# Kernel optimization log

Hardware: AMD Instinct MI355X
Metric: run time of the kernel (lower is better)

## Reference

```python
import jax, jax.numpy as jnp
import numpy as np


def setup_inputs() -> dict:
    key = jax.random.key(0)
    k1, k2 = jax.random.split(key)
    x = jax.random.normal(k1, (32, 112, 112, 64), dtype=jnp.float32)
    kernels = jax.random.normal(k2, (3, 3, 64, 128), dtype=jnp.float32) * 0.05
    biases = jnp.zeros((128,), dtype=jnp.float32)
    return {"x": x, "kernels": kernels, "biases": biases}


def reference(x, kernels, biases):
    # Stride-1 VALID cross-correlation, NHWC input, HWIO kernel -> NHWC output.
    # Matches the original's per-pixel sum(patch * kernel) over all input channels.
    out = jax.lax.conv_general_dilated(
        x, kernels,
        window_strides=(1, 1),
        padding="VALID",
        dimension_numbers=("NHWC", "HWIO", "NHWC"),
    )
    out = out + biases  # broadcast over (B, H_out, W_out, F)
    return jax.nn.relu(out)  # activation=relu per init_kwargs
```

## Files before the change

kernel.cpp:

```cpp
#include <hip/hip_runtime.h>
#include <hip/hip_bf16.h>

typedef __attribute__((ext_vector_type(4))) float f32x4;
typedef __attribute__((ext_vector_type(8))) short bf16x8;
typedef __attribute__((ext_vector_type(8))) unsigned short u16x8;

#define NB 32
#define HH 112
#define WW 112
#define CIN 64
#define COUT 128
#define HOUT 110
#define WOUT 110

__device__ __forceinline__ unsigned short f2bf(float f) {
  unsigned int x = __float_as_uint(f);
  x += 0x7fffu + ((x >> 16) & 1u);
  return (unsigned short)(x >> 16);
}

__global__ void prepack_b_kernel(const float* __restrict__ kern,
                                 unsigned short* __restrict__ bt) {
  int idx = blockIdx.x * 256 + threadIdx.x;
  if (idx >= 576 * COUT) return;
  int co = idx / 576;
  int k = idx - co * 576;
  bt[idx] = f2bf(kern[k * COUT + co]);
}

template <bool PREPACK>
__global__ __launch_bounds__(512)
void conv_mfma_kernel(const float* __restrict__ x,
                      const void* __restrict__ bsrc,
                      const float* __restrict__ bias,
                      float* __restrict__ out) {
  __shared__ __align__(16) unsigned short As[128 * 64];
  __shared__ __align__(16) unsigned short Bs[128 * 64];

  const int tid = threadIdx.x;
  const int m0 = blockIdx.x * 128;

  const int sr = tid >> 2;
  const int sc = tid & 3;
  const int m = m0 + sr;
  const int wo = m % WOUT;
  const int t1 = m / WOUT;
  const int ho = t1 % HOUT;
  const int b = t1 / HOUT;
  const float* xrow = x + (((b * HH) + ho) * WW + wo) * CIN + sc * 16;
  const int swzS = (sr & 7) << 4;
  unsigned short* aw0 = As + sr * 64 + ((((sc * 32) + 0) ^ swzS) >> 1);
  unsigned short* aw1 = As + sr * 64 + ((((sc * 32) + 16) ^ swzS) >> 1);

  const unsigned short* btrow = nullptr;
  unsigned short* bw0 = nullptr;
  unsigned short* bw1 = nullptr;
  if constexpr (PREPACK) {
    btrow = (const unsigned short*)bsrc + sr * 576 + sc * 16;
    bw0 = Bs + sr * 64 + ((((sc * 32) + 0) ^ swzS) >> 1);
    bw1 = Bs + sr * 64 + ((((sc * 32) + 16) ^ swzS) >> 1);
  }
  const int bci = tid >> 3;
  const int bco = (tid & 7) * 16;

  const int lane = tid & 63;
  const int wid = tid >> 6;
  const int wm = wid >> 1;
  const int wn = wid & 1;
  const int l16 = lane & 15;
  const int lk = lane >> 4;
  const int swzR = (l16 & 7) << 4;

  f32x4 acc[2][4];
#pragma unroll
  for (int i = 0; i < 2; ++i)
#pragma unroll
    for (int j = 0; j < 4; ++j)
      acc[i][j] = (f32x4){0.f, 0.f, 0.f, 0.f};

  const unsigned short* ar0 = As + (wm * 32 + 0 + l16) * 64;
  const unsigned short* ar1 = As + (wm * 32 + 16 + l16) * 64;
  const unsigned short* br0 = Bs + (wn * 64 + 0 + l16) * 64;
  const unsigned short* br1 = Bs + (wn * 64 + 16 + l16) * 64;
  const unsigned short* br2 = Bs + (wn * 64 + 32 + l16) * 64;
  const unsigned short* br3 = Bs + (wn * 64 + 48 + l16) * 64;

  for (int kk = 0; kk < 9; ++kk) {
    const int kh = kk / 3;
    const int kw = kk - kh * 3;

    __syncthreads();

    {
      const float* src = xrow + (kh * WW + kw) * CIN;
      f32x4 f0 = *(const f32x4*)(src + 0);
      f32x4 f1 = *(const f32x4*)(src + 4);
      f32x4 f2 = *(const f32x4*)(src + 8);
      f32x4 f3 = *(const f32x4*)(src + 12);
      u16x8 v0, v1;
#pragma unroll
      for (int j = 0; j < 4; ++j) {
        v0[j]     = f2bf(f0[j]);
        v0[4 + j] = f2bf(f1[j]);
        v1[j]     = f2bf(f2[j]);
        v1[4 + j] = f2bf(f3[j]);
      }
      *(u16x8*)aw0 = v0;
      *(u16x8*)aw1 = v1;
    }

    if constexpr (PREPACK) {
      const u16x8* p = (const u16x8*)(btrow + kk * 64);
      *(u16x8*)bw0 = p[0];
      *(u16x8*)bw1 = p[1];
    } else {
      const float* kern = (const float*)bsrc;
      const float* ks = kern + (kk * 64 + bci) * COUT + bco;
      f32x4 g0 = *(const f32x4*)(ks + 0);
      f32x4 g1 = *(const f32x4*)(ks + 4);
      f32x4 g2 = *(const f32x4*)(ks + 8);
      f32x4 g3 = *(const f32x4*)(ks + 12);
#pragma unroll
      for (int j = 0; j < 4; ++j) {
        int c0 = bco + j;
        Bs[c0 * 64 + (((bci * 2) ^ ((c0 & 7) << 4)) >> 1)] = f2bf(g0[j]);
        int c1 = bco + 4 + j;
        Bs[c1 * 64 + (((bci * 2) ^ ((c1 & 7) << 4)) >> 1)] = f2bf(g1[j]);
        int c2 = bco + 8 + j;
        Bs[c2 * 64 + (((bci * 2) ^ ((c2 & 7) << 4)) >> 1)] = f2bf(g2[j]);
        int c3 = bco + 12 + j;
        Bs[c3 * 64 + (((bci * 2) ^ ((c3 & 7) << 4)) >> 1)] = f2bf(g3[j]);
      }
    }

    __syncthreads();

#pragma unroll
    for (int ks = 0; ks < 2; ++ks) {
      const int cbs = ((ks * 64 + lk * 16) ^ swzR) >> 1;
      bf16x8 a0 = *(const bf16x8*)(ar0 + cbs);
      bf16x8 a1 = *(const bf16x8*)(ar1 + cbs);
      bf16x8 b0 = *(const bf16x8*)(br0 + cbs);
      bf16x8 b1 = *(const bf16x8*)(br1 + cbs);
      bf16x8 b2 = *(const bf16x8*)(br2 + cbs);
      bf16x8 b3 = *(const bf16x8*)(br3 + cbs);
      acc[0][0] = __builtin_amdgcn_mfma_f32_16x16x32_bf16(a0, b0, acc[0][0], 0, 0, 0);
      acc[0][1] = __builtin_amdgcn_mfma_f32_16x16x32_bf16(a0, b1, acc[0][1], 0, 0, 0);
      acc[0][2] = __builtin_amdgcn_mfma_f32_16x16x32_bf16(a0, b2, acc[0][2], 0, 0, 0);
      acc[0][3] = __builtin_amdgcn_mfma_f32_16x16x32_bf16(a0, b3, acc[0][3], 0, 0, 0);
      acc[1][0] = __builtin_amdgcn_mfma_f32_16x16x32_bf16(a1, b0, acc[1][0], 0, 0, 0);
      acc[1][1] = __builtin_amdgcn_mfma_f32_16x16x32_bf16(a1, b1, acc[1][1], 0, 0, 0);
      acc[1][2] = __builtin_amdgcn_mfma_f32_16x16x32_bf16(a1, b2, acc[1][2], 0, 0, 0);
      acc[1][3] = __builtin_amdgcn_mfma_f32_16x16x32_bf16(a1, b3, acc[1][3], 0, 0, 0);
    }
  }

  const int ncol = wn * 64 + l16;
  const float bv0 = bias[ncol + 0];
  const float bv1 = bias[ncol + 16];
  const float bv2 = bias[ncol + 32];
  const float bv3 = bias[ncol + 48];
  const int mrow0 = m0 + wm * 32 + lk * 4;
#pragma unroll
  for (int mf = 0; mf < 2; ++mf) {
#pragma unroll
    for (int j = 0; j < 4; ++j) {
      const int row = mrow0 + mf * 16 + j;
      float* orow = out + (size_t)row * COUT + ncol;
      orow[0]  = fmaxf(acc[mf][0][j] + bv0, 0.f);
      orow[16] = fmaxf(acc[mf][1][j] + bv1, 0.f);
      orow[32] = fmaxf(acc[mf][2][j] + bv2, 0.f);
      orow[48] = fmaxf(acc[mf][3][j] + bv3, 0.f);
    }
  }
}

extern "C" void kernel_launch(void* const* d_in, const int* in_sizes, int n_in,
                              void* d_out, int out_size, void* d_ws, size_t ws_size,
                              hipStream_t stream) {
  const float* x = (const float*)d_in[0];
  const float* kern = (const float*)d_in[1];
  const float* bias = (const float*)d_in[2];
  float* out = (float*)d_out;

  const size_t bt_bytes = 576 * COUT * sizeof(unsigned short);
  if (d_ws != nullptr && ws_size >= bt_bytes) {
    unsigned short* bt = (unsigned short*)d_ws;
    prepack_b_kernel<<<288, 256, 0, stream>>>(kern, bt);
    conv_mfma_kernel<true><<<3025, 512, 0, stream>>>(x, (const void*)bt, bias, out);
  } else {
    conv_mfma_kernel<false><<<3025, 512, 0, stream>>>(x, (const void*)kern, bias, out);
  }
}
```

Measured before the change: 114.8 us.

## Double-buffer LDS tiles and prefetch next tap's loads during MFMA

Splits the A and B shared-memory tiles into two buffers and issues the global loads for the next kernel tap before the MFMA block on the current tap. The next buffer is converted and stored after the compute, leaving one barrier per iteration instead of two. The aim is to hide global load latency behind matrix math. In exchange it doubles LDS use to 64KB per block and raises register pressure, which may lower occupancy.

Result: faster. 110.4 us (-3.9%).

```diff
diff --git a/kernel.cpp b/kernel.cpp
--- a/kernel.cpp
+++ b/kernel.cpp
@@ -12,6 +12,7 @@
 #define COUT 128
 #define HOUT 110
 #define WOUT 110
+#define NWG 3025
 
 __device__ __forceinline__ unsigned short f2bf(float f) {
   unsigned int x = __float_as_uint(f);
@@ -34,8 +35,8 @@
                       const void* __restrict__ bsrc,
                       const float* __restrict__ bias,
                       float* __restrict__ out) {
-  __shared__ __align__(16) unsigned short As[128 * 64];
-  __shared__ __align__(16) unsigned short Bs[128 * 64];
+  __shared__ __align__(16) unsigned short As[2][128 * 64];
+  __shared__ __align__(16) unsigned short Bs[2][128 * 64];
 
   const int tid = threadIdx.x;
   const int m0 = blockIdx.x * 128;
@@ -49,16 +50,12 @@
   const int b = t1 / HOUT;
   const float* xrow = x + (((b * HH) + ho) * WW + wo) * CIN + sc * 16;
   const int swzS = (sr & 7) << 4;
-  unsigned short* aw0 = As + sr * 64 + ((((sc * 32) + 0) ^ swzS) >> 1);
-  unsigned short* aw1 = As + sr * 64 + ((((sc * 32) + 16) ^ swzS) >> 1);
+  const int awoff0 = sr * 64 + ((((sc * 32) + 0) ^ swzS) >> 1);
+  const int awoff1 = sr * 64 + ((((sc * 32) + 16) ^ swzS) >> 1);
 
   const unsigned short* btrow = nullptr;
-  unsigned short* bw0 = nullptr;
-  unsigned short* bw1 = nullptr;
   if constexpr (PREPACK) {
     btrow = (const unsigned short*)bsrc + sr * 576 + sc * 16;
-    bw0 = Bs + sr * 64 + ((((sc * 32) + 0) ^ swzS) >> 1);
-    bw1 = Bs + sr * 64 + ((((sc * 32) + 16) ^ swzS) >> 1);
   }
   const int bci = tid >> 3;
   const int bco = (tid & 7) * 16;
@@ -71,6 +68,13 @@
   const int lk = lane >> 4;
   const int swzR = (l16 & 7) << 4;
 
+  const int aroff0 = (wm * 32 + 0 + l16) * 64;
+  const int aroff1 = (wm * 32 + 16 + l16) * 64;
+  const int broff0 = (wn * 64 + 0 + l16) * 64;
+  const int broff1 = (wn * 64 + 16 + l16) * 64;
+  const int broff2 = (wn * 64 + 32 + l16) * 64;
+  const int broff3 = (wn * 64 + 48 + l16) * 64;
+
   f32x4 acc[2][4];
 #pragma unroll
   for (int i = 0; i < 2; ++i)
@@ -78,72 +82,82 @@
     for (int j = 0; j < 4; ++j)
       acc[i][j] = (f32x4){0.f, 0.f, 0.f, 0.f};
 
-  const unsigned short* ar0 = As + (wm * 32 + 0 + l16) * 64;
-  const unsigned short* ar1 = As + (wm * 32 + 16 + l16) * 64;
-  const unsigned short* br0 = Bs + (wn * 64 + 0 + l16) * 64;
-  const unsigned short* br1 = Bs + (wn * 64 + 16 + l16) * 64;
-  const unsigned short* br2 = Bs + (wn * 64 + 32 + l16) * 64;
-  const unsigned short* br3 = Bs + (wn * 64 + 48 + l16) * 64;
-
-  for (int kk = 0; kk < 9; ++kk) {
-    const int kh = kk / 3;
-    const int kw = kk - kh * 3;
-
-    __syncthreads();
-
-    {
-      const float* src = xrow + (kh * WW + kw) * CIN;
-      f32x4 f0 = *(const f32x4*)(src + 0);
-      f32x4 f1 = *(const f32x4*)(src + 4);
-      f32x4 f2 = *(const f32x4*)(src + 8);
-      f32x4 f3 = *(const f32x4*)(src + 12);
-      u16x8 v0, v1;
-#pragma unroll
-      for (int j = 0; j < 4; ++j) {
-        v0[j]     = f2bf(f0[j]);
-        v0[4 + j] = f2bf(f1[j]);
-        v1[j]     = f2bf(f2[j]);
-        v1[4 + j] = f2bf(f3[j]);
-      }
-      *(u16x8*)aw0 = v0;
-      *(u16x8*)aw1 = v1;
-    }
-
+  {
+    f32x4 f0 = *(const f32x4*)(xrow + 0);
+    f32x4 f1 = *(const f32x4*)(xrow + 4);
+    f32x4 f2 = *(const f32x4*)(xrow + 8);
+    f32x4 f3 = *(const f32x4*)(xrow + 12);
+    u16x8 v0, v1;
+#pragma unroll
+    for (int j = 0; j < 4; ++j) {
+      v0[j]     = f2bf(f0[j]);
+      v0[4 + j] = f2bf(f1[j]);
+      v1[j]     = f2bf(f2[j]);
+      v1[4 + j] = f2bf(f3[j]);
+    }
+    *(u16x8*)(As[0] + awoff0) = v0;
+    *(u16x8*)(As[0] + awoff1) = v1;
     if constexpr (PREPACK) {
-      const u16x8* p = (const u16x8*)(btrow + kk * 64);
-      *(u16x8*)bw0 = p[0];
-      *(u16x8*)bw1 = p[1];
+      const u16x8* p = (const u16x8*)btrow;
+      *(u16x8*)(Bs[0] + awoff0) = p[0];
+      *(u16x8*)(Bs[0] + awoff1) = p[1];
     } else {
       const float* kern = (const float*)bsrc;
-      const float* ks = kern + (kk * 64 + bci) * COUT + bco;
-      f32x4 g0 = *(const f32x4*)(ks + 0);
-      f32x4 g1 = *(const f32x4*)(ks + 4);
-      f32x4 g2 = *(const f32x4*)(ks + 8);
-      f32x4 g3 = *(const f32x4*)(ks + 12);
+      const float* kslab = kern + bci * COUT + bco;
+      f32x4 g0 = *(const f32x4*)(kslab + 0);
+      f32x4 g1 = *(const f32x4*)(kslab + 4);
+      f32x4 g2 = *(const f32x4*)(kslab + 8);
+      f32x4 g3 = *(const f32x4*)(kslab + 12);
 #pragma unroll
       for (int j = 0; j < 4; ++j) {
         int c0 = bco + j;
-        Bs[c0 * 64 + (((bci * 2) ^ ((c0 & 7) << 4)) >> 1)] = f2bf(g0[j]);
+        Bs[0][c0 * 64 + (((bci * 2) ^ ((c0 & 7) << 4)) >> 1)] = f2bf(g0[j]);
         int c1 = bco + 4 + j;
-        Bs[c1 * 64 + (((bci * 2) ^ ((c1 & 7) << 4)) >> 1)] = f2bf(g1[j]);
+        Bs[0][c1 * 64 + (((bci * 2) ^ ((c1 & 7) << 4)) >> 1)] = f2bf(g1[j]);
         int c2 = bco + 8 + j;
-        Bs[c2 * 64 + (((bci * 2) ^ ((c2 & 7) << 4)) >> 1)] = f2bf(g2[j]);
+        Bs[0][c2 * 64 + (((bci * 2) ^ ((c2 & 7) << 4)) >> 1)] = f2bf(g2[j]);
         int c3 = bco + 12 + j;
-        Bs[c3 * 64 + (((bci * 2) ^ ((c3 & 7) << 4)) >> 1)] = f2bf(g3[j]);
+        Bs[0][c3 * 64 + (((bci * 2) ^ ((c3 & 7) << 4)) >> 1)] = f2bf(g3[j]);
+      }
+    }
+  }
+
+#pragma unroll
+  for (int kk = 0; kk < 9; ++kk) {
+    const int cur = kk & 1;
+    const int nxt = cur ^ 1;
+
+    f32x4 g0, g1, g2, g3;
+    u16x8 bq0, bq1;
+    if (kk < 8) {
+      const int kn = kk + 1;
+      const int kh2 = kn / 3;
+      const int kw2 = kn - kh2 * 3;
+      const float* src = xrow + (kh2 * WW + kw2) * CIN;
+      g0 = *(const f32x4*)(src + 0);
+      g1 = *(const f32x4*)(src + 4);
+      g2 = *(const f32x4*)(src + 8);
+      g3 = *(const f32x4*)(src + 12);
+      if constexpr (PREPACK) {
+        const u16x8* p = (const u16x8*)(btrow + kn * 64);
+        bq0 = p[0];
+        bq1 = p[1];
       }
     }
 
     __syncthreads();
 
+    const unsigned short* Ac = As[cur];
+    const unsigned short* Bc = Bs[cur];
 #pragma unroll
     for (int ks = 0; ks < 2; ++ks) {
       const int cbs = ((ks * 64 + lk * 16) ^ swzR) >> 1;
-      bf16x8 a0 = *(const bf16x8*)(ar0 + cbs);
-      bf16x8 a1 = *(const bf16x8*)(ar1 + cbs);
-      bf16x8 b0 = *(const bf16x8*)(br0 + cbs);
-      bf16x8 b1 = *(const bf16x8*)(br1 + cbs);
-      bf16x8 b2 = *(const bf16x8*)(br2 + cbs);
-      bf16x8 b3 = *(const bf16x8*)(br3 + cbs);
+      bf16x8 a0 = *(const bf16x8*)(Ac + aroff0 + cbs);
+      bf16x8 a1 = *(const bf16x8*)(Ac + aroff1 + cbs);
+      bf16x8 b0 = *(const bf16x8*)(Bc + broff0 + cbs);
+      bf16x8 b1 = *(const bf16x8*)(Bc + broff1 + cbs);
+      bf16x8 b2 = *(const bf16x8*)(Bc + broff2 + cbs);
+      bf16x8 b3 = *(const bf16x8*)(Bc + broff3 + cbs);
       acc[0][0] = __builtin_amdgcn_mfma_f32_16x16x32_bf16(a0, b0, acc[0][0], 0, 0, 0);
       acc[0][1] = __builtin_amdgcn_mfma_f32_16x16x32_bf16(a0, b1, acc[0][1], 0, 0, 0);
       acc[0][2] = __builtin_amdgcn_mfma_f32_16x16x32_bf16(a0, b2, acc[0][2], 0, 0, 0);
@@ -153,6 +167,41 @@
       acc[1][2] = __builtin_amdgcn_mfma_f32_16x16x32_bf16(a1, b2, acc[1][2], 0, 0, 0);
       acc[1][3] = __builtin_amdgcn_mfma_f32_16x16x32_bf16(a1, b3, acc[1][3], 0, 0, 0);
     }
+
+    if (kk < 8) {
+      u16x8 v0, v1;
+#pragma unroll
+      for (int j = 0; j < 4; ++j) {
+        v0[j]     = f2bf(g0[j]);
+        v0[4 + j] = f2bf(g1[j]);
+        v1[j]     = f2bf(g2[j]);
+        v1[4 + j] = f2bf(g3[j]);
+      }
+      *(u16x8*)(As[nxt] + awoff0) = v0;
+      *(u16x8*)(As[nxt] + awoff1) = v1;
+      if constexpr (PREPACK) {
+        *(u16x8*)(Bs[nxt] + awoff0) = bq0;
+        *(u16x8*)(Bs[nxt] + awoff1) = bq1;
+      } else {
+        const float* kern = (const float*)bsrc;
+        const float* kslab = kern + ((kk + 1) * 64 + bci) * COUT + bco;
+        f32x4 h0 = *(const f32x4*)(kslab + 0);
+        f32x4 h1 = *(const f32x4*)(kslab + 4);
+        f32x4 h2 = *(const f32x4*)(kslab + 8);
+        f32x4 h3 = *(const f32x4*)(kslab + 12);
+#pragma unroll
+        for (int j = 0; j < 4; ++j) {
+          int c0 = bco + j;
+          Bs[nxt][c0 * 64 + (((bci * 2) ^ ((c0 & 7) << 4)) >> 1)] = f2bf(h0[j]);
+          int c1 = bco + 4 + j;
+          Bs[nxt][c1 * 64 + (((bci * 2) ^ ((c1 & 7) << 4)) >> 1)] = f2bf(h1[j]);
+          int c2 = bco + 8 + j;
+          Bs[nxt][c2 * 64 + (((bci * 2) ^ ((c2 & 7) << 4)) >> 1)] = f2bf(h2[j]);
+          int c3 = bco + 12 + j;
+          Bs[nxt][c3 * 64 + (((bci * 2) ^ ((c3 & 7) << 4)) >> 1)] = f2bf(h3[j]);
+        }
+      }
+    }
   }
 
   const int ncol = wn * 64 + l16;
@@ -187,8 +236,8 @@
   if (d_ws != nullptr && ws_size >= bt_bytes) {
     unsigned short* bt = (unsigned short*)d_ws;
     prepack_b_kernel<<<288, 256, 0, stream>>>(kern, bt);
-    conv_mfma_kernel<true><<<3025, 512, 0, stream>>>(x, (const void*)bt, bias, out);
+    conv_mfma_kernel<true><<<NWG, 512, 0, stream>>>(x, (const void*)bt, bias, out);
   } else {
-    conv_mfma_kernel<false><<<3025, 512, 0, stream>>>(x, (const void*)kern, bias, out);
-  }
-}
+    conv_mfma_kernel<false><<<NWG, 512, 0, stream>>>(x, (const void*)kern, bias, out);
+  }
+}
```

## Switch to 32x32x16 MFMA with 256-thread blocks and XCD-aware block remap

Applied to the files above, without the earlier changes.

Moves from 16x16x32 to 32x32x16 bf16 MFMA tiles, with each of 4 waves computing a 64x64 sub-tile. Blocks shrink to 256 threads that each load twice as much A/B data per K step. Block indices are remapped so consecutive M tiles land on the same XCD for L2 locality. The conversion uses a packed bf16x2 intrinsic and the K loop is fully unrolled. This raises per-wave MFMA efficiency and reduces LDS reads per FLOP, at the cost of more registers and fewer waves per block.

Result: slower. 174.7 us (+52.1%).

```diff
diff --git a/kernel.cpp b/kernel.cpp
--- a/kernel.cpp
+++ b/kernel.cpp
@@ -2,21 +2,31 @@
 #include <hip/hip_bf16.h>
 
 typedef __attribute__((ext_vector_type(4))) float f32x4;
+typedef __attribute__((ext_vector_type(16))) float f32x16;
 typedef __attribute__((ext_vector_type(8))) short bf16x8;
 typedef __attribute__((ext_vector_type(8))) unsigned short u16x8;
-
-#define NB 32
+typedef __attribute__((ext_vector_type(4))) unsigned int u32x4;
+
 #define HH 112
 #define WW 112
 #define CIN 64
 #define COUT 128
 #define HOUT 110
 #define WOUT 110
+#define MTOT 387200
+#define NWG 3025
+#define NXCD 8
 
 __device__ __forceinline__ unsigned short f2bf(float f) {
   unsigned int x = __float_as_uint(f);
   x += 0x7fffu + ((x >> 16) & 1u);
   return (unsigned short)(x >> 16);
+}
+
+__device__ __forceinline__ unsigned int cvt2(float lo, float hi) {
+  union { __hip_bfloat162 h; unsigned int u; } cv;
+  cv.h = __float22bfloat162_rn(float2{lo, hi});
+  return cv.u;
 }
 
 __global__ void prepack_b_kernel(const float* __restrict__ kern,
@@ -29,7 +39,7 @@
 }
 
 template <bool PREPACK>
-__global__ __launch_bounds__(512)
+__global__ __launch_bounds__(256, 3)
 void conv_mfma_kernel(const float* __restrict__ x,
                       const void* __restrict__ bsrc,
                       const float* __restrict__ bias,
@@ -38,53 +48,54 @@
   __shared__ __align__(16) unsigned short Bs[128 * 64];
 
   const int tid = threadIdx.x;
-  const int m0 = blockIdx.x * 128;
-
-  const int sr = tid >> 2;
-  const int sc = tid & 3;
+
+  const int bid = blockIdx.x;
+  const int q = NWG / NXCD, r = NWG % NXCD;
+  const int xcd = bid % NXCD, i8 = bid / NXCD;
+  const int wg = (xcd < r ? xcd * (q + 1) : r * (q + 1) + (xcd - r) * q) + i8;
+  const int m0 = wg * 128;
+
+  const int sr = tid >> 1;
+  const int sc = tid & 1;
   const int m = m0 + sr;
   const int wo = m % WOUT;
   const int t1 = m / WOUT;
   const int ho = t1 % HOUT;
   const int b = t1 / HOUT;
-  const float* xrow = x + (((b * HH) + ho) * WW + wo) * CIN + sc * 16;
+  const float* xrow = x + (((b * HH) + ho) * WW + wo) * CIN + sc * 32;
   const int swzS = (sr & 7) << 4;
-  unsigned short* aw0 = As + sr * 64 + ((((sc * 32) + 0) ^ swzS) >> 1);
-  unsigned short* aw1 = As + sr * 64 + ((((sc * 32) + 16) ^ swzS) >> 1);
+  int awo[4];
+#pragma unroll
+  for (int i = 0; i < 4; ++i)
+    awo[i] = sr * 64 + (((sc * 64 + i * 16) ^ swzS) >> 1);
 
   const unsigned short* btrow = nullptr;
-  unsigned short* bw0 = nullptr;
-  unsigned short* bw1 = nullptr;
   if constexpr (PREPACK) {
-    btrow = (const unsigned short*)bsrc + sr * 576 + sc * 16;
-    bw0 = Bs + sr * 64 + ((((sc * 32) + 0) ^ swzS) >> 1);
-    bw1 = Bs + sr * 64 + ((((sc * 32) + 16) ^ swzS) >> 1);
-  }
-  const int bci = tid >> 3;
-  const int bco = (tid & 7) * 16;
+    btrow = (const unsigned short*)bsrc + sr * 576 + sc * 32;
+  }
+  const int fci = tid >> 2;
+  const int fco = (tid & 3) * 32;
 
   const int lane = tid & 63;
   const int wid = tid >> 6;
   const int wm = wid >> 1;
   const int wn = wid & 1;
-  const int l16 = lane & 15;
-  const int lk = lane >> 4;
-  const int swzR = (l16 & 7) << 4;
-
-  f32x4 acc[2][4];
-#pragma unroll
-  for (int i = 0; i < 2; ++i)
-#pragma unroll
-    for (int j = 0; j < 4; ++j)
-      acc[i][j] = (f32x4){0.f, 0.f, 0.f, 0.f};
-
-  const unsigned short* ar0 = As + (wm * 32 + 0 + l16) * 64;
-  const unsigned short* ar1 = As + (wm * 32 + 16 + l16) * 64;
-  const unsigned short* br0 = Bs + (wn * 64 + 0 + l16) * 64;
-  const unsigned short* br1 = Bs + (wn * 64 + 16 + l16) * 64;
-  const unsigned short* br2 = Bs + (wn * 64 + 32 + l16) * 64;
-  const unsigned short* br3 = Bs + (wn * 64 + 48 + l16) * 64;
-
+  const int l31 = lane & 31;
+  const int hi = lane >> 5;
+  const int hi16 = hi * 16;
+  const int swzC = (l31 & 7) << 4;
+
+  const int arow0 = (wm * 64 + 0 + l31) * 64;
+  const int arow1 = (wm * 64 + 32 + l31) * 64;
+  const int bcol0 = (wn * 64 + 0 + l31) * 64;
+  const int bcol1 = (wn * 64 + 32 + l31) * 64;
+
+  f32x16 acc00 = {};
+  f32x16 acc01 = {};
+  f32x16 acc10 = {};
+  f32x16 acc11 = {};
+
+#pragma unroll
   for (int kk = 0; kk < 9; ++kk) {
     const int kh = kk / 3;
     const int kw = kk - kh * 3;
@@ -97,80 +108,77 @@
       f32x4 f1 = *(const f32x4*)(src + 4);
       f32x4 f2 = *(const f32x4*)(src + 8);
       f32x4 f3 = *(const f32x4*)(src + 12);
-      u16x8 v0, v1;
-#pragma unroll
-      for (int j = 0; j < 4; ++j) {
-        v0[j]     = f2bf(f0[j]);
-        v0[4 + j] = f2bf(f1[j]);
-        v1[j]     = f2bf(f2[j]);
-        v1[4 + j] = f2bf(f3[j]);
-      }
-      *(u16x8*)aw0 = v0;
-      *(u16x8*)aw1 = v1;
+      f32x4 f4 = *(const f32x4*)(src + 16);
+      f32x4 f5 = *(const f32x4*)(src + 20);
+      f32x4 f6 = *(const f32x4*)(src + 24);
+      f32x4 f7 = *(const f32x4*)(src + 28);
+      u32x4 v0, v1, v2, v3;
+      v0[0] = cvt2(f0[0], f0[1]); v0[1] = cvt2(f0[2], f0[3]);
+      v0[2] = cvt2(f1[0], f1[1]); v0[3] = cvt2(f1[2], f1[3]);
+      v1[0] = cvt2(f2[0], f2[1]); v1[1] = cvt2(f2[2], f2[3]);
+      v1[2] = cvt2(f3[0], f3[1]); v1[3] = cvt2(f3[2], f3[3]);
+      v2[0] = cvt2(f4[0], f4[1]); v2[1] = cvt2(f4[2], f4[3]);
+      v2[2] = cvt2(f5[0], f5[1]); v2[3] = cvt2(f5[2], f5[3]);
+      v3[0] = cvt2(f6[0], f6[1]); v3[1] = cvt2(f6[2], f6[3]);
+      v3[2] = cvt2(f7[0], f7[1]); v3[3] = cvt2(f7[2], f7[3]);
+      *(u32x4*)(As + awo[0]) = v0;
+      *(u32x4*)(As + awo[1]) = v1;
+      *(u32x4*)(As + awo[2]) = v2;
+      *(u32x4*)(As + awo[3]) = v3;
     }
 
     if constexpr (PREPACK) {
-      const u16x8* p = (const u16x8*)(btrow + kk * 64);
-      *(u16x8*)bw0 = p[0];
-      *(u16x8*)bw1 = p[1];
+      const u16x8* s = (const u16x8*)(btrow + kk * 64);
+      *(u16x8*)(Bs + awo[0]) = s[0];
+      *(u16x8*)(Bs + awo[1]) = s[1];
+      *(u16x8*)(Bs + awo[2]) = s[2];
+      *(u16x8*)(Bs + awo[3]) = s[3];
     } else {
       const float* kern = (const float*)bsrc;
-      const float* ks = kern + (kk * 64 + bci) * COUT + bco;
-      f32x4 g0 = *(const f32x4*)(ks + 0);
-      f32x4 g1 = *(const f32x4*)(ks + 4);
-      f32x4 g2 = *(const f32x4*)(ks + 8);
-      f32x4 g3 = *(const f32x4*)(ks + 12);
-#pragma unroll
-      for (int j = 0; j < 4; ++j) {
-        int c0 = bco + j;
-        Bs[c0 * 64 + (((bci * 2) ^ ((c0 & 7) << 4)) >> 1)] = f2bf(g0[j]);
-        int c1 = bco + 4 + j;
-        Bs[c1 * 64 + (((bci * 2) ^ ((c1 & 7) << 4)) >> 1)] = f2bf(g1[j]);
-        int c2 = bco + 8 + j;
-        Bs[c2 * 64 + (((bci * 2) ^ ((c2 & 7) << 4)) >> 1)] = f2bf(g2[j]);
-        int c3 = bco + 12 + j;
-        Bs[c3 * 64 + (((bci * 2) ^ ((c3 & 7) << 4)) >> 1)] = f2bf(g3[j]);
+      const float* kslab = kern + (kk * 64 + fci) * COUT + fco;
+#pragma unroll
+      for (int j = 0; j < 32; ++j) {
+        int c = fco + j;
+        Bs[c * 64 + (((fci * 2) ^ ((c & 7) << 4)) >> 1)] = f2bf(kslab[j]);
       }
     }
 
     __syncthreads();
 
 #pragma unroll
-    for (int ks = 0; ks < 2; ++ks) {
-      const int cbs = ((ks * 64 + lk * 16) ^ swzR) >> 1;
-      bf16x8 a0 = *(const bf16x8*)(ar0 + cbs);
-      bf16x8 a1 = *(const bf16x8*)(ar1 + cbs);
-      bf16x8 b0 = *(const bf16x8*)(br0 + cbs);
-      bf16x8 b1 = *(const bf16x8*)(br1 + cbs);
-      bf16x8 b2 = *(const bf16x8*)(br2 + cbs);
-      bf16x8 b3 = *(const bf16x8*)(br3 + cbs);
-      acc[0][0] = __builtin_amdgcn_mfma_f32_16x16x32_bf16(a0, b0, acc[0][0], 0, 0, 0);
-      acc[0][1] = __builtin_amdgcn_mfma_f32_16x16x32_bf16(a0, b1, acc[0][1], 0, 0, 0);
-      acc[0][2] = __builtin_amdgcn_mfma_f32_16x16x32_bf16(a0, b2, acc[0][2], 0, 0, 0);
-      acc[0][3] = __builtin_amdgcn_mfma_f32_16x16x32_bf16(a0, b3, acc[0][3], 0, 0, 0);
-      acc[1][0] = __builtin_amdgcn_mfma_f32_16x16x32_bf16(a1, b0, acc[1][0], 0, 0, 0);
-      acc[1][1] = __builtin_amdgcn_mfma_f32_16x16x32_bf16(a1, b1, acc[1][1], 0, 0, 0);
-      acc[1][2] = __builtin_amdgcn_mfma_f32_16x16x32_bf16(a1, b2, acc[1][2], 0, 0, 0);
-      acc[1][3] = __builtin_amdgcn_mfma_f32_16x16x32_bf16(a1, b3, acc[1][3], 0, 0, 0);
-    }
-  }
-
-  const int ncol = wn * 64 + l16;
-  const float bv0 = bias[ncol + 0];
-  const float bv1 = bias[ncol + 16];
-  const float bv2 = bias[ncol + 32];
-  const float bv3 = bias[ncol + 48];
-  const int mrow0 = m0 + wm * 32 + lk * 4;
-#pragma unroll
-  for (int mf = 0; mf < 2; ++mf) {
+    for (int ks = 0; ks < 4; ++ks) {
+      const int coff = ((ks * 32 + hi16) ^ swzC) >> 1;
+      bf16x8 a0 = *(const bf16x8*)(As + arow0 + coff);
+      bf16x8 a1 = *(const bf16x8*)(As + arow1 + coff);
+      bf16x8 b0 = *(const bf16x8*)(Bs + bcol0 + coff);
+      bf16x8 b1 = *(const bf16x8*)(Bs + bcol1 + coff);
+      acc00 = __builtin_amdgcn_mfma_f32_32x32x16_bf16(a0, b0, acc00, 0, 0, 0);
+      acc01 = __builtin_amdgcn_mfma_f32_32x32x16_bf16(a0, b1, acc01, 0, 0, 0);
+      acc10 = __builtin_amdgcn_mfma_f32_32x32x16_bf16(a1, b0, acc10, 0, 0, 0);
+      acc11 = __builtin_amdgcn_mfma_f32_32x32x16_bf16(a1, b1, acc11, 0, 0, 0);
+    }
+  }
+
+  const int col0 = wn * 64 + l31;
+  const float bv0 = bias[col0];
+  const float bv1 = bias[col0 + 32];
+  const int rbase = m0 + wm * 64 + hi * 4;
+#pragma unroll
+  for (int qd = 0; qd < 4; ++qd) {
 #pragma unroll
     for (int j = 0; j < 4; ++j) {
-      const int row = mrow0 + mf * 16 + j;
-      float* orow = out + (size_t)row * COUT + ncol;
-      orow[0]  = fmaxf(acc[mf][0][j] + bv0, 0.f);
-      orow[16] = fmaxf(acc[mf][1][j] + bv1, 0.f);
-      orow[32] = fmaxf(acc[mf][2][j] + bv2, 0.f);
-      orow[48] = fmaxf(acc[mf][3][j] + bv3, 0.f);
+      const int rloc = j + qd * 8;
+      const int e = qd * 4 + j;
+      {
+        float* o = out + (size_t)(rbase + rloc) * COUT + col0;
+        o[0]  = fmaxf(acc00[e] + bv0, 0.f);
+        o[32] = fmaxf(acc01[e] + bv1, 0.f);
+      }
+      {
+        float* o = out + (size_t)(rbase + 32 + rloc) * COUT + col0;
+        o[0]  = fmaxf(acc10[e] + bv0, 0.f);
+        o[32] = fmaxf(acc11[e] + bv1, 0.f);
+      }
     }
   }
 }
@@ -187,8 +195,8 @@
   if (d_ws != nullptr && ws_size >= bt_bytes) {
     unsigned short* bt = (unsigned short*)d_ws;
     prepack_b_kernel<<<288, 256, 0, stream>>>(kern, bt);
-    conv_mfma_kernel<true><<<3025, 512, 0, stream>>>(x, (const void*)bt, bias, out);
+    conv_mfma_kernel<true><<<NWG, 256, 0, stream>>>(x, (const void*)bt, bias, out);
   } else {
-    conv_mfma_kernel<false><<<3025, 512, 0, stream>>>(x, (const void*)kern, bias, out);
-  }
-}
+    conv_mfma_kernel<false><<<NWG, 256, 0, stream>>>(x, (const void*)kern, bias, out);
+  }
+}
```
